# Performance work log

Hardware: AMD Instinct MI355X
Metric: run time of the kernel (lower is better)

Reference implementation:

```python
import jax, jax.numpy as jnp
import numpy as np
import math

B, T, D = 2, 1024, 256
N, H = 1024, 8
HD = N // H
K = 32
STEPS = 2
VOCAB = 32000
TWO_PI = 2.0 * math.pi


def _ln(x, g, b):
    mu = x.mean(-1, keepdims=True)
    var = ((x - mu) ** 2).mean(-1, keepdims=True)
    return (x - mu) / jnp.sqrt(var + 1e-5) * g + b


def _gelu(x):
    # torch nn.GELU default = exact erf form
    return jax.nn.gelu(x, approximate=False)


def _forward(tokens, emb, field_init, Wq, Wv, mW1, mb1, mW2, mb2, base_metric,
             decoder, hebbian, fW1, fb1, fW2, fb2, g1, b1, g2, b2, gf, bf, Wl, bl):
    x = emb[tokens] + field_init  # [B,T,D]
    # quantized RoPE (BDH): freqs quantized in pairs, phases mod 1
    freqs = 1.0 / (2.0 ** 16) ** (jnp.floor(jnp.arange(D) / 2) * 2.0 / D) / TWO_PI  # [D]
    phases = (jnp.arange(T, dtype=jnp.float32)[:, None] * freqs[None, :]) % 1.0 * TWO_PI  # [T,D]
    cos, sin = jnp.cos(phases)[None], jnp.sin(phases)[None]
    x_rot = jnp.stack([-x[..., 1::2], x[..., ::2]], axis=-1).reshape(x.shape)
    x = x * cos + x_rot * sin

    # window j of token t covers padded positions t..t+K-1 == original t-(K-1)..t (causal)
    win_idx = jnp.arange(T)[:, None] + jnp.arange(K)[None, :]  # [T,K]

    def interaction(y):
        qs = jax.nn.relu(jnp.einsum('btd,hde->bthe', y, Wq))  # [B,T,H,HD] sparse query
        vs = jax.nn.relu(jnp.einsum('btd,hde->bthe', y, Wv))  # [B,T,H,HD] sparse value
        # dynamic diagonal metric from field signature
        qf = qs.reshape(B, T, N)
        sig = qf.mean(1) + qf[:, ::8].mean(1) * 0.5  # T >= 8 branch
        mod = _gelu(sig @ mW1 + mb1) @ mW2 + mb2  # [B,H*HD]
        metric = jax.nn.softplus(base_metric[None] + 0.1 * mod.reshape(B, H, HD)) + 1e-6
        # causal k-window extraction (unfold equivalent)
        qp = jnp.pad(qs, ((0, 0), (K - 1, 0), (0, 0), (0, 0)))
        vp = jnp.pad(vs, ((0, 0), (K - 1, 0), (0, 0), (0, 0)))
        qw = qp[:, win_idx].transpose(0, 1, 3, 2, 4)  # [B,T,H,K,HD]
        vw = vp[:, win_idx].transpose(0, 1, 3, 2, 4)
        diff = qs[:, :, :, None, :] - qw
        dist = jnp.sqrt(jnp.sum(metric[:, None, :, None, :] * diff ** 2, -1) + 1e-8)  # [B,T,H,K]
        infl = jnp.exp(-dist)
        infl = infl / (infl.sum(-1, keepdims=True) + 1e-8)
        ctx = jnp.einsum('bthk,bthkd->bthd', infl, vw)
        # Hebbian memory contraction (eval mode: state is fixed buffer)
        qn = qs / jnp.maximum(jnp.linalg.norm(qs, axis=-1, keepdims=True), 1e-12)
        ctx = ctx + jnp.einsum('bthd,hde->bthe', qn, hebbian)
        # multiplicative gating + decode
        return (qs * ctx).reshape(B, T, N) @ decoder

    for _ in range(STEPS):  # fixed evolution steps (eval, dropout off)
        dx = interaction(_ln(x, g1, b1)) + (_gelu(_ln(x, g2, b2) @ fW1 + fb1) @ fW2 + fb2)
        x = x + dx
    return _ln(x, gf, bf) @ Wl + bl  # [B,T,VOCAB]


def setup_inputs() -> dict:
    key = jax.random.key(0)
    ks = jax.random.split(key, 12)
    s = 0.02
    return {
        'tokens': jax.random.randint(ks[0], (B, T), 0, VOCAB),
        'emb': jax.random.normal(ks[1], (VOCAB, D)) * s,
        'field_init': jax.random.normal(ks[2], (1, 1, D)) * s,
        'Wq': jax.random.normal(ks[3], (H, D, HD)) * s,
        'Wv': jax.random.normal(ks[4], (H, D, HD)) * s,
        'mW1': jax.random.normal(ks[5], (N, N // 2)) * s,
        'mb1': jnp.zeros((N // 2,)),
        'mW2': jax.random.normal(ks[6], (N // 2, H * HD)) * s,
        'mb2': jnp.zeros((H * HD,)),
        'base_metric': jnp.ones((H, HD)) * 0.1,
        'decoder': jax.random.normal(ks[7], (N, D)) * s,
        'hebbian': jax.random.normal(ks[8], (H, HD, HD)) * 0.01,
        'fW1': jax.random.normal(ks[9], (D, 4 * D)) * s,
        'fb1': jnp.zeros((4 * D,)),
        'fW2': jax.random.normal(ks[10], (4 * D, D)) * s,
        'fb2': jnp.zeros((D,)),
        'g1': jnp.ones((D,)), 'b1': jnp.zeros((D,)),
        'g2': jnp.ones((D,)), 'b2': jnp.zeros((D,)),
        'gf': jnp.ones((D,)), 'bf': jnp.zeros((D,)),
        'Wl': jax.random.normal(ks[11], (D, VOCAB)) * s,
        'bl': jnp.zeros((VOCAB,)),
    }


def reference(tokens, emb, field_init, Wq, Wv, mW1, mb1, mW2, mb2, base_metric,
              decoder, hebbian, fW1, fb1, fW2, fb2, g1, b1, g2, b2, gf, bf, Wl, bl):
    return _forward(tokens, emb, field_init, Wq, Wv, mW1, mb1, mW2, mb2, base_metric,
                    decoder, hebbian, fW1, fb1, fW2, fb2, g1, b1, g2, b2, gf, bf, Wl, bl)
```

## Files before the change

### kernel.cpp

```cpp
#include <hip/hip_runtime.h>
#include <hip/hip_bf16.h>
#include <math.h>

#define B_ 2
#define T_ 1024
#define D_ 256
#define N_ 1024
#define H_ 8
#define HD_ 128
#define K_ 32
#define VOCAB_ 32000

typedef __attribute__((ext_vector_type(8))) short short8v;
typedef __attribute__((ext_vector_type(4))) float f32x4;

static __device__ __forceinline__ float geluf(float x) {
    return 0.5f * x * (1.0f + erff(x * 0.70710678118654752f));
}

static __device__ __forceinline__ ushort f2bf(float f) {
    unsigned u = __builtin_bit_cast(unsigned, f);
    u += 0x7fff + ((u >> 16) & 1);
    return (ushort)(u >> 16);
}

static __device__ __forceinline__ float bf2f(ushort u) {
    unsigned v = ((unsigned)u) << 16;
    return __builtin_bit_cast(float, v);
}

__global__ void embed_rope_ln_kernel(const int* __restrict__ tokens,
                                     const float* __restrict__ emb,
                                     const float* __restrict__ field_init,
                                     const float* __restrict__ g1, const float* __restrict__ b1,
                                     const float* __restrict__ g2, const float* __restrict__ b2,
                                     float* __restrict__ x,
                                     ushort* __restrict__ y1, ushort* __restrict__ y2) {
    int bt = blockIdx.x;
    int d = threadIdx.x;
    int t = bt & (T_ - 1);
    int tok = tokens[bt];
    float v = emb[(long)tok * D_ + d] + field_init[d];
    float partner = __shfl_xor(v, 1);
    float rot = (d & 1) ? partner : -partner;
    float freq = exp2f(-0.0625f * (float)(d & ~1)) * (1.0f / 6.283185307179586f);
    float ph = fmodf((float)t * freq, 1.0f) * 6.283185307179586f;
    v = v * cosf(ph) + rot * sinf(ph);
    long i = (long)bt * D_ + d;
    x[i] = v;
    __shared__ float red[4];
    int lane = d & 63, wid = d >> 6;
    float s = v;
    #pragma unroll
    for (int off = 32; off; off >>= 1) s += __shfl_xor(s, off);
    if (lane == 0) red[wid] = s;
    __syncthreads();
    float mu = (red[0] + red[1] + red[2] + red[3]) * (1.0f / D_);
    float dv = v - mu;
    float s2 = dv * dv;
    #pragma unroll
    for (int off = 32; off; off >>= 1) s2 += __shfl_xor(s2, off);
    __syncthreads();
    if (lane == 0) red[wid] = s2;
    __syncthreads();
    float var = (red[0] + red[1] + red[2] + red[3]) * (1.0f / D_);
    float rstd = rsqrtf(var + 1e-5f);
    float nv = dv * rstd;
    y1[i] = f2bf(nv * g1[d] + b1[d]);
    y2[i] = f2bf(nv * g2[d] + b2[d]);
}

__global__ void ln_kernel(float* __restrict__ x,
                          const float* __restrict__ addA, const float* __restrict__ addB,
                          const float* __restrict__ g1, const float* __restrict__ b1,
                          const float* __restrict__ g2, const float* __restrict__ b2,
                          ushort* __restrict__ y1, ushort* __restrict__ y2) {
    int row = blockIdx.x;
    int d = threadIdx.x;
    long i = (long)row * D_ + d;
    float v = x[i] + addA[i] + addB[i];
    x[i] = v;
    __shared__ float red[4];
    int lane = d & 63, wid = d >> 6;
    float s = v;
    #pragma unroll
    for (int off = 32; off; off >>= 1) s += __shfl_xor(s, off);
    if (lane == 0) red[wid] = s;
    __syncthreads();
    float mu = (red[0] + red[1] + red[2] + red[3]) * (1.0f / D_);
    float dv = v - mu;
    float s2 = dv * dv;
    #pragma unroll
    for (int off = 32; off; off >>= 1) s2 += __shfl_xor(s2, off);
    __syncthreads();
    if (lane == 0) red[wid] = s2;
    __syncthreads();
    float var = (red[0] + red[1] + red[2] + red[3]) * (1.0f / D_);
    float rstd = rsqrtf(var + 1e-5f);
    float nv = dv * rstd;
    y1[i] = f2bf(nv * g1[d] + b1[d]);
    if (y2) y2[i] = f2bf(nv * g2[d] + b2[d]);
}

static __device__ __forceinline__ void tcast_tile(
    const float* __restrict__ in, ushort* __restrict__ out,
    int R, int C, int ry, int cx) {
    __shared__ float sm[64][65];
    int r0 = ry * 64, c0 = cx * 64;
    int tx = threadIdx.x & 63, ty = threadIdx.x >> 6;
    #pragma unroll
    for (int i = 0; i < 16; ++i) {
        int r = i * 4 + ty;
        sm[r][tx] = in[(long)(r0 + r) * C + c0 + tx];
    }
    __syncthreads();
    #pragma unroll
    for (int i = 0; i < 16; ++i) {
        int c = i * 4 + ty;
        out[(long)(c0 + c) * R + r0 + tx] = f2bf(sm[tx][c]);
    }
}

__global__ __launch_bounds__(256) void tcast_kernel(
    const float* __restrict__ in, ushort* __restrict__ out, int R, int C) {
    tcast_tile(in, out, R, C, blockIdx.y, blockIdx.x);
}

struct TcastBatch {
    const float* in[8];
    ushort* out[8];
    long inS[8], outS[8];
    int cb[8], rb[8], R[8], C[8];
    int cum[9];
};

__global__ __launch_bounds__(256) void tcast_all_kernel(TcastBatch tb) {
    int bid = blockIdx.x;
    int d = 0;
    #pragma unroll
    for (int i = 0; i < 8; ++i) if (bid >= tb.cum[i + 1]) d = i + 1;
    int local = bid - tb.cum[d];
    int bpz = tb.cb[d] * tb.rb[d];
    int z = local / bpz;
    int rem = local - z * bpz;
    int cx = rem % tb.cb[d], ry = rem / tb.cb[d];
    tcast_tile(tb.in[d] + z * tb.inS[d], tb.out[d] + z * tb.outS[d],
               tb.R[d], tb.C[d], ry, cx);
}

#define LDK 72
#define CSTR 132

template<int ACT, int OUTBF, int SIG>
__device__ __forceinline__ void gemm128_core(
    const ushort* __restrict__ A, int lda,
    const ushort* __restrict__ Bt, int ldb,
    const float* __restrict__ bias, void* __restrict__ Cout, int ldc,
    int Kd, int bx, int by,
    float* __restrict__ psOut, float* __restrict__ ps8Out) {
    __shared__ __align__(16) ushort As[128 * LDK];
    __shared__ __align__(16) ushort Bs[128 * LDK];
    int tid = threadIdx.x;
    int wid = tid >> 6, lane = tid & 63;
    int brow = by * 128, bcol = bx * 128;
    int wr = wid >> 1, wc = wid & 1;
    f32x4 acc[4][4] = {};
    for (int k0 = 0; k0 < Kd; k0 += 64) {
        __syncthreads();
        #pragma unroll
        for (int j = 0; j < 4; ++j) {
            int idx = tid + j * 256;
            int r = idx >> 3, sgm = idx & 7;
            *(short8v*)&As[r * LDK + sgm * 8] =
                *(const short8v*)&A[(long)(brow + r) * lda + k0 + sgm * 8];
            *(short8v*)&Bs[r * LDK + sgm * 8] =
                *(const short8v*)&Bt[(long)(bcol + r) * ldb + k0 + sgm * 8];
        }
        __syncthreads();
        #pragma unroll
        for (int kk = 0; kk < 2; ++kk) {
            short8v af[4], bfv[4];
            #pragma unroll
            for (int m = 0; m < 4; ++m)
                af[m] = *(const short8v*)&As[(wr * 64 + m * 16 + (lane & 15)) * LDK + kk * 32 + (lane >> 4) * 8];
            #pragma unroll
            for (int n = 0; n < 4; ++n)
                bfv[n] = *(const short8v*)&Bs[(wc * 64 + n * 16 + (lane & 15)) * LDK + kk * 32 + (lane >> 4) * 8];
            #pragma unroll
            for (int m = 0; m < 4; ++m)
                #pragma unroll
                for (int n = 0; n < 4; ++n)
                    acc[m][n] = __builtin_amdgcn_mfma_f32_16x16x32_bf16(af[m], bfv[n], acc[m][n], 0, 0, 0);
        }
    }
    float* Cs = (float*)As;
    float cs = 0.f, cs8 = 0.f;
    #pragma unroll
    for (int chunk = 0; chunk < 4; ++chunk) {
        __syncthreads();
        if (wr == (chunk >> 1)) {
            #pragma unroll
            for (int mm = 0; mm < 2; ++mm) {
                int m = (chunk & 1) * 2 + mm;
                int lr0 = mm * 16 + ((lane >> 4) << 2);
                #pragma unroll
                for (int n = 0; n < 4; ++n) {
                    int lcol = wc * 64 + n * 16 + (lane & 15);
                    #pragma unroll
                    for (int j = 0; j < 4; ++j)
                        Cs[(lr0 + j) * CSTR + lcol] = acc[m][n][j];
                }
            }
        }
        __syncthreads();
        int lrow = tid >> 3, f4 = tid & 7;
        long grow = brow + chunk * 32 + lrow;
        if (OUTBF) {
            #pragma unroll
            for (int u = 0; u < 2; ++u) {
                int c0i = (f4 + u * 8) * 8;
                uint pk[4];
                #pragma unroll
                for (int q = 0; q < 4; ++q) {
                    int cc = c0i + 2 * q;
                    float v0 = Cs[lrow * CSTR + cc]     + (bias ? bias[bcol + cc] : 0.0f);
                    float v1 = Cs[lrow * CSTR + cc + 1] + (bias ? bias[bcol + cc + 1] : 0.0f);
                    if (ACT == 1) { v0 = fmaxf(v0, 0.0f); v1 = fmaxf(v1, 0.0f); }
                    else if (ACT == 2) { v0 = geluf(v0); v1 = geluf(v1); }
                    pk[q] = (uint)f2bf(v0) | ((uint)f2bf(v1) << 16);
                }
                *(uint4*)&((ushort*)Cout)[grow * ldc + bcol + c0i] = *(uint4*)pk;
            }
        } else {
            #pragma unroll
            for (int u = 0; u < 4; ++u) {
                int c0i = (f4 + u * 8) * 4;
                float vv[4];
                #pragma unroll
                for (int q = 0; q < 4; ++q) {
                    float v = Cs[lrow * CSTR + c0i + q] + (bias ? bias[bcol + c0i + q] : 0.0f);
                    if (ACT == 1) v = fmaxf(v, 0.0f);
                    else if (ACT == 2) v = geluf(v);
                    vv[q] = v;
                }
                *(float4*)&((float*)Cout)[grow * ldc + bcol + c0i] = *(float4*)vv;
            }
        }
        if (SIG && tid < 128) {
            #pragma unroll
            for (int r = 0; r < 32; ++r) {
                float vr = fmaxf(Cs[r * CSTR + tid], 0.0f);
                cs += vr;
                if ((r & 7) == 0) cs8 += vr;
            }
        }
    }
    if (SIG && tid < 128) {
        psOut[by * 1024 + bcol + tid] = cs;
        ps8Out[by * 1024 + bcol + tid] = cs8;
    }
}

__global__ __launch_bounds__(256) void gemm3_kernel(
    const ushort* __restrict__ y1, const ushort* __restrict__ y2,
    const ushort* __restrict__ WqT, const ushort* __restrict__ WvT, const ushort* __restrict__ fW1T,
    const float* __restrict__ fb1,
    ushort* __restrict__ qs, ushort* __restrict__ vs, ushort* __restrict__ ffnh,
    float* __restrict__ ps, float* __restrict__ ps8) {
    int z = blockIdx.z;
    if (z == 0)
        gemm128_core<1, 1, 1>(y1, 256, WqT, 256, nullptr, qs, 1024, 256,
                              blockIdx.x, blockIdx.y, ps, ps8);
    else if (z == 1)
        gemm128_core<1, 1, 0>(y1, 256, WvT, 256, nullptr, vs, 1024, 256,
                              blockIdx.x, blockIdx.y, nullptr, nullptr);
    else
        gemm128_core<2, 1, 0>(y2, 256, fW1T, 256, fb1, ffnh, 1024, 256,
                              blockIdx.x, blockIdx.y, nullptr, nullptr);
}

__global__ __launch_bounds__(256) void vocab_kernel(
    const ushort* __restrict__ yf, const ushort* __restrict__ WlT,
    const float* __restrict__ bl, float* __restrict__ out) {
    int g = blockIdx.x;
    int nid = (g & 7) * 500 + (g >> 3);
    gemm128_core<0, 0, 0>(yf, 256, WlT, 256, bl, out, VOCAB_, 256,
                          nid >> 4, nid & 15, nullptr, nullptr);
}

__global__ __launch_bounds__(256) void gemm2_kernel(
    const ushort* __restrict__ gated, const ushort* __restrict__ ffnh,
    const ushort* __restrict__ decT, const ushort* __restrict__ fW2T,
    const float* __restrict__ fb2,
    float* __restrict__ dec_out, float* __restrict__ ffn_out) {
    int z = blockIdx.z;
    const ushort* A = z ? ffnh : gated;
    const ushort* Bt = z ? fW2T : decT;
    const float* bias = z ? fb2 : nullptr;
    float* C = z ? ffn_out : dec_out;
    const int Kd = 1024, N = 256;
    __shared__ __align__(16) ushort As[64 * LDK];
    __shared__ __align__(16) ushort Bs[64 * LDK];
    int tid = threadIdx.x;
    int wid = tid >> 6, lane = tid & 63;
    int brow = blockIdx.y * 64, bcol = blockIdx.x * 64;
    int wr = wid >> 1, wc = wid & 1;
    f32x4 acc[2][2] = {};
    for (int k0 = 0; k0 < Kd; k0 += 64) {
        __syncthreads();
        #pragma unroll
        for (int j = 0; j < 2; ++j) {
            int idx = tid + j * 256;
            int r = idx >> 3, sgm = idx & 7;
            *(short8v*)&As[r * LDK + sgm * 8] =
                *(const short8v*)&A[(long)(brow + r) * Kd + k0 + sgm * 8];
            *(short8v*)&Bs[r * LDK + sgm * 8] =
                *(const short8v*)&Bt[(long)(bcol + r) * Kd + k0 + sgm * 8];
        }
        __syncthreads();
        #pragma unroll
        for (int kk = 0; kk < 2; ++kk) {
            short8v af[2], bfv[2];
            #pragma unroll
            for (int m = 0; m < 2; ++m)
                af[m] = *(const short8v*)&As[(wr * 32 + m * 16 + (lane & 15)) * LDK + kk * 32 + (lane >> 4) * 8];
            #pragma unroll
            for (int n = 0; n < 2; ++n)
                bfv[n] = *(const short8v*)&Bs[(wc * 32 + n * 16 + (lane & 15)) * LDK + kk * 32 + (lane >> 4) * 8];
            #pragma unroll
            for (int m = 0; m < 2; ++m)
                #pragma unroll
                for (int n = 0; n < 2; ++n)
                    acc[m][n] = __builtin_amdgcn_mfma_f32_16x16x32_bf16(af[m], bfv[n], acc[m][n], 0, 0, 0);
        }
    }
    int r0 = brow + wr * 32 + ((lane >> 4) << 2);
    int c0 = bcol + wc * 32 + (lane & 15);
    #pragma unroll
    for (int n = 0; n < 2; ++n) {
        int col = c0 + n * 16;
        float bv = bias ? bias[col] : 0.0f;
        #pragma unroll
        for (int m = 0; m < 2; ++m)
            #pragma unroll
            for (int j = 0; j < 4; ++j)
                C[(long)(r0 + m * 16 + j) * N + col] = acc[m][n][j] + bv;
    }
}

__global__ __launch_bounds__(256) void mlp1_kernel(
    const float* __restrict__ ps, const float* __restrict__ ps8,
    const ushort* __restrict__ mW1T, const float* __restrict__ mb1,
    float* __restrict__ hid) {
    int blk = blockIdx.x;
    int b = blk >> 7;
    __shared__ float sig_l[1024];
    int tid = threadIdx.x;
    for (int c = tid; c < 1024; c += 256) {
        float s = 0.f, s8 = 0.f;
        #pragma unroll
        for (int by8 = 0; by8 < 8; ++by8) {
            s += ps[(b * 8 + by8) * 1024 + c];
            s8 += ps8[(b * 8 + by8) * 1024 + c];
        }
        sig_l[c] = s * (1.0f / 1024.0f) + 0.5f * s8 * (1.0f / 128.0f);
    }
    __syncthreads();
    int wv = tid >> 6, lane = tid & 63;
    int j = (blk & 127) * 4 + wv;
    const ushort* wrow = mW1T + (long)j * 1024;
    float acc = 0.f;
    #pragma unroll
    for (int c2 = 0; c2 < 4; ++c2) {
        int n0 = c2 * 256 + lane * 4;
        float4 sv = *(const float4*)&sig_l[n0];
        ushort4 w4 = *(const ushort4*)&wrow[n0];
        acc += bf2f(w4.x) * sv.x + bf2f(w4.y) * sv.y
             + bf2f(w4.z) * sv.z + bf2f(w4.w) * sv.w;
    }
    #pragma unroll
    for (int off = 32; off; off >>= 1) acc += __shfl_xor(acc, off);
    if (lane == 0) hid[b * 512 + j] = geluf(acc + mb1[j]);
}

__global__ __launch_bounds__(256) void mlp2_kernel(
    const float* __restrict__ hid, const ushort* __restrict__ mW2T,
    const float* __restrict__ mb2, const float* __restrict__ base_metric,
    float* __restrict__ metric) {
    int widx = blockIdx.x * 4 + (threadIdx.x >> 6);
    int b = widx >> 10, i = widx & 1023;
    int lane = threadIdx.x & 63;
    const float* hd = hid + b * 512;
    const ushort* w = mW2T + (long)i * 512;
    int j0 = lane * 8;
    short8v wv = *(const short8v*)&w[j0];
    float4 h0 = *(const float4*)&hd[j0];
    float4 h1 = *(const float4*)&hd[j0 + 4];
    float acc = bf2f((ushort)wv[0]) * h0.x + bf2f((ushort)wv[1]) * h0.y
              + bf2f((ushort)wv[2]) * h0.z + bf2f((ushort)wv[3]) * h0.w
              + bf2f((ushort)wv[4]) * h1.x + bf2f((ushort)wv[5]) * h1.y
              + bf2f((ushort)wv[6]) * h1.z + bf2f((ushort)wv[7]) * h1.w;
    #pragma unroll
    for (int off = 32; off; off >>= 1) acc += __shfl_xor(acc, off);
    if (lane == 0) {
        float v = base_metric[i] + 0.1f * (acc + mb2[i]);
        float sp = fmaxf(v, 0.f) + log1pf(expf(-fabsf(v)));
        metric[b * 1024 + i] = sp + 1e-6f;
    }
}

#define QLD 136
#define QLDU 68
#define VLD 72
#define PLD 72
#define CLD 132

__global__ __launch_bounds__(256) void window_kernel(
    const ushort* __restrict__ qs, const ushort* __restrict__ vs,
    const float* __restrict__ metric, const ushort* __restrict__ hebT,
    ushort* __restrict__ gated) {
    int tile = blockIdx.x, h = blockIdx.y, b = blockIdx.z;
    int t0 = tile * 16;
    int tid = threadIdx.x;
    __shared__ __align__(16) ushort Qt[48 * QLD];
    __shared__ __align__(16) ushort Qr[16 * QLD];
    __shared__ __align__(16) ushort Vt[128 * VLD];
    __shared__ __align__(16) ushort P[16 * PLD];
    __shared__ float ctx[16 * CLD];
    __shared__ float ns[48], invn_l[16], part[3][16], smf[128];

    if (tid < 128) smf[tid] = sqrtf(metric[(b * H_ + h) * HD_ + tid]);
    if (tid < 128) { int t = tid >> 3, c = tid & 7; ((uint*)P)[t * 36 + 24 + c] = 0; }
    __syncthreads();

    for (int i = tid; i < 48 * 64; i += 256) {
        int r = i >> 6, c = i & 63;
        int grow = t0 - 31 + r;
        uint qv = 0;
        if (r < 47 && grow >= 0)
            qv = ((const uint*)qs)[(((long)(b * T_ + grow) * N_ + h * HD_) >> 1) + c];
        float q0 = bf2f((ushort)(qv & 0xffff)) * smf[2 * c];
        float q1 = bf2f((ushort)(qv >> 16)) * smf[2 * c + 1];
        ((uint*)Qt)[r * QLDU + c] = (uint)f2bf(q0) | ((uint)f2bf(q1) << 16);
        if (r >= 31 && r < 47) ((uint*)Qr)[(r - 31) * QLDU + c] = qv;
    }
    for (int i = tid; i < 32 * 64; i += 256) {
        int r2 = i >> 6, c = i & 63;
        int ra = 2 * r2, rb_ = 2 * r2 + 1;
        int ga = t0 - 31 + ra, gb = t0 - 31 + rb_;
        uint v0 = 0, v1 = 0;
        if (ra < 47 && ga >= 0)
            v0 = ((const uint*)vs)[(((long)(b * T_ + ga) * N_ + h * HD_) >> 1) + c];
        if (rb_ < 47 && gb >= 0)
            v1 = ((const uint*)vs)[(((long)(b * T_ + gb) * N_ + h * HD_) >> 1) + c];
        ((uint*)Vt)[(2 * c) * 36 + r2]     = (v0 & 0xffff) | ((v1 & 0xffff) << 16);
        ((uint*)Vt)[(2 * c + 1) * 36 + r2] = (v0 >> 16) | (v1 & 0xffff0000u);
    }
    __syncthreads();

    int w = tid >> 6, lane = tid & 63;
    int lc = lane & 15, lr = lane >> 4;

    for (int rr = 0; rr < 16; ++rr) {
        int row = w * 16 + rr;
        uint u = (row < 48) ? ((uint*)Qt)[row * QLDU + lane]
                            : ((uint*)Qr)[(row - 48) * QLDU + lane];
        float a0 = bf2f((ushort)(u & 0xffff)), a1 = bf2f((ushort)(u >> 16));
        float nv = a0 * a0 + a1 * a1;
        #pragma unroll
        for (int off = 32; off; off >>= 1) nv += __shfl_xor(nv, off);
        if (lane == 0) {
            if (row < 48) ns[row] = nv;
            else invn_l[row - 48] = 1.0f / fmaxf(sqrtf(nv), 1e-12f);
        }
    }
    __syncthreads();

    f32x4 accS = {};
    if (w < 3) {
        #pragma unroll
        for (int k = 0; k < 4; ++k) {
            short8v a = *(const short8v*)&Qt[(w * 16 + lc) * QLD + k * 32 + lr * 8];
            short8v bf_ = *(const short8v*)&Qt[(31 + lc) * QLD + k * 32 + lr * 8];
            accS = __builtin_amdgcn_mfma_f32_16x16x32_bf16(a, bf_, accS, 0, 0, 0);
        }
    }
    f32x4 accH[2] = {};
    const ushort* hb = hebT + (long)h * HD_ * HD_;
    #pragma unroll
    for (int nt = 0; nt < 2; ++nt)
        #pragma unroll
        for (int k = 0; k < 4; ++k) {
            short8v a = *(const short8v*)&Qr[lc * QLD + k * 32 + lr * 8];
            short8v bf_ = *(const short8v*)&hb[(long)((w * 2 + nt) * 16 + lc) * HD_ + k * 32 + lr * 8];
            accH[nt] = __builtin_amdgcn_mfma_f32_16x16x32_bf16(a, bf_, accH[nt], 0, 0, 0);
        }
    #pragma unroll
    for (int nt = 0; nt < 2; ++nt)
        #pragma unroll
        for (int j = 0; j < 4; ++j) {
            int t = lr * 4 + j;
            ctx[t * CLD + (w * 2 + nt) * 16 + lc] = accH[nt][j] * invn_l[t];
        }
    float wgt[4];
    if (w < 3) {
        float nt_ = ns[31 + lc];
        float psum = 0.f;
        #pragma unroll
        for (int j = 0; j < 4; ++j) {
            int s = w * 16 + lr * 4 + j;
            float val = fmaxf(nt_ + ns[s] - 2.0f * accS[j], 0.0f) + 1e-8f;
            bool band = (s >= lc) && (s <= lc + 31);
            wgt[j] = band ? __expf(-sqrtf(val)) : 0.0f;
            psum += wgt[j];
        }
        psum += __shfl_xor(psum, 16);
        psum += __shfl_xor(psum, 32);
        if (lane < 16) part[w][lane] = psum;
    }
    __syncthreads();
    if (w < 3) {
        float inv = 1.0f / (part[0][lc] + part[1][lc] + part[2][lc] + 1e-8f);
        uint lo = (uint)f2bf(wgt[0] * inv) | ((uint)f2bf(wgt[1] * inv) << 16);
        uint hi = (uint)f2bf(wgt[2] * inv) | ((uint)f2bf(wgt[3] * inv) << 16);
        uint2 pk = {lo, hi};
        *(uint2*)&P[lc * PLD + w * 16 + lr * 4] = pk;
    }
    __syncthreads();
    f32x4 accP[2] = {};
    #pragma unroll
    for (int mt = 0; mt < 2; ++mt)
        #pragma unroll
        for (int k = 0; k < 2; ++k) {
            short8v a = *(const short8v*)&Vt[((w * 2 + mt) * 16 + lc) * VLD + k * 32 + lr * 8];
            short8v bf_ = *(const short8v*)&P[lc * PLD + k * 32 + lr * 8];
            accP[mt] = __builtin_amdgcn_mfma_f32_16x16x32_bf16(a, bf_, accP[mt], 0, 0, 0);
        }
    #pragma unroll
    for (int mt = 0; mt < 2; ++mt)
        #pragma unroll
        for (int j = 0; j < 4; ++j) {
            int e = (w * 2 + mt) * 16 + lr * 4 + j;
            ctx[lc * CLD + e] += accP[mt][j];
        }
    __syncthreads();
    {
        int t = tid >> 4, g = tid & 15;
        uint4 qu = *(const uint4*)&((const uint*)Qr)[t * QLDU + g * 4];
        const float* crow = &ctx[t * CLD + g * 8];
        uint qa[4] = {qu.x, qu.y, qu.z, qu.w};
        uint outp[4];
        #pragma unroll
        for (int q4 = 0; q4 < 4; ++q4) {
            float e0 = bf2f((ushort)(qa[q4] & 0xffff)) * crow[2 * q4];
            float e1 = bf2f((ushort)(qa[q4] >> 16))   * crow[2 * q4 + 1];
            outp[q4] = (uint)f2bf(e0) | ((uint)f2bf(e1) << 16);
        }
        *(uint4*)&gated[(long)(b * T_ + t0 + t) * N_ + h * HD_ + g * 8] = *(uint4*)outp;
    }
}

extern "C" void kernel_launch(void* const* d_in, const int* in_sizes, int n_in,
                              void* d_out, int out_size, void* d_ws, size_t ws_size,
                              hipStream_t stream) {
    const int*   tokens      = (const int*)  d_in[0];
    const float* emb         = (const float*)d_in[1];
    const float* field_init  = (const float*)d_in[2];
    const float* Wq          = (const float*)d_in[3];
    const float* Wv          = (const float*)d_in[4];
    const float* mW1         = (const float*)d_in[5];
    const float* mb1         = (const float*)d_in[6];
    const float* mW2         = (const float*)d_in[7];
    const float* mb2         = (const float*)d_in[8];
    const float* base_metric = (const float*)d_in[9];
    const float* decoder     = (const float*)d_in[10];
    const float* hebbian     = (const float*)d_in[11];
    const float* fW1         = (const float*)d_in[12];
    const float* fb1         = (const float*)d_in[13];
    const float* fW2         = (const float*)d_in[14];
    const float* fb2         = (const float*)d_in[15];
    const float* g1          = (const float*)d_in[16];
    const float* b1          = (const float*)d_in[17];
    const float* g2          = (const float*)d_in[18];
    const float* b2          = (const float*)d_in[19];
    const float* gf          = (const float*)d_in[20];
    const float* bf          = (const float*)d_in[21];
    const float* Wl          = (const float*)d_in[22];
    const float* bl          = (const float*)d_in[23];
    float* out = (float*)d_out;

    char* wp = (char*)d_ws;
    auto alloc = [&](size_t bytes) { char* p = wp; wp += (bytes + 255) & ~255UL; return p; };
    float*  x        = (float*) alloc(524288 * 4);
    ushort* y1_bf    = (ushort*)alloc(524288 * 2);
    ushort* y2_bf    = (ushort*)alloc(524288 * 2);
    ushort* yf_bf    = (ushort*)alloc(524288 * 2);
    ushort* qs_bf    = (ushort*)alloc(2097152 * 2);
    ushort* vs_bf    = (ushort*)alloc(2097152 * 2);
    ushort* gated_bf = (ushort*)alloc(2097152 * 2);
    ushort* ffnh_bf  = (ushort*)alloc(2097152 * 2);
    float*  dec_out  = (float*) alloc(524288 * 4);
    float*  ffn_out  = (float*) alloc(524288 * 4);
    ushort* WqT      = (ushort*)alloc(262144 * 2);
    ushort* WvT      = (ushort*)alloc(262144 * 2);
    ushort* decT     = (ushort*)alloc(262144 * 2);
    ushort* fW1T     = (ushort*)alloc(262144 * 2);
    ushort* fW2T     = (ushort*)alloc(262144 * 2);
    ushort* mW1T     = (ushort*)alloc(524288 * 2);
    ushort* mW2T     = (ushort*)alloc(524288 * 2);
    ushort* hebT     = (ushort*)alloc(131072 * 2);
    float*  ps       = (float*) alloc(16 * 1024 * 4);
    float*  ps8      = (float*) alloc(16 * 1024 * 4);
    float*  hid      = (float*) alloc(1024 * 4);
    float*  metricb  = (float*) alloc(2048 * 4);
    ushort* WlT      = (ushort*)qs_bf;

    TcastBatch tb;
    const float* tin[8]  = {Wq, Wv, decoder, fW1, fW2, mW1, mW2, hebbian};
    ushort*      tout[8] = {WqT, WvT, decT, fW1T, fW2T, mW1T, mW2T, hebT};
    long tinS[8]  = {256 * 128, 256 * 128, 0, 0, 0, 0, 0, 128 * 128};
    long toutS[8] = {128 * 256, 128 * 256, 0, 0, 0, 0, 0, 128 * 128};
    int tR[8] = {256, 256, 1024, 256, 1024, 1024, 512, 128};
    int tC[8] = {128, 128, 256, 1024, 256, 512, 1024, 128};
    int cum = 0;
    tb.cum[0] = 0;
    for (int i = 0; i < 8; ++i) {
        tb.in[i] = tin[i]; tb.out[i] = tout[i];
        tb.inS[i] = tinS[i]; tb.outS[i] = toutS[i];
        tb.R[i] = tR[i]; tb.C[i] = tC[i];
        tb.cb[i] = tC[i] / 64; tb.rb[i] = tR[i] / 64;
        int zc = (i == 0 || i == 1 || i == 7) ? 8 : 1;
        cum += tb.cb[i] * tb.rb[i] * zc;
        tb.cum[i + 1] = cum;
    }
    tcast_all_kernel<<<cum, 256, 0, stream>>>(tb);

    embed_rope_ln_kernel<<<B_ * T_, 256, 0, stream>>>(
        tokens, emb, field_init, g1, b1, g2, b2, x, y1_bf, y2_bf);

    for (int step = 0; step < 2; ++step) {
        if (step == 1)
            ln_kernel<<<B_ * T_, 256, 0, stream>>>(
                x, dec_out, ffn_out, g1, b1, g2, b2, y1_bf, y2_bf);
        gemm3_kernel<<<dim3(8, 16, 3), 256, 0, stream>>>(
            y1_bf, y2_bf, WqT, WvT, fW1T, fb1, qs_bf, vs_bf, ffnh_bf, ps, ps8);
        mlp1_kernel<<<256, 256, 0, stream>>>(ps, ps8, mW1T, mb1, hid);
        mlp2_kernel<<<512, 256, 0, stream>>>(hid, mW2T, mb2, base_metric, metricb);
        window_kernel<<<dim3(T_ / 16, H_, B_), 256, 0, stream>>>(
            qs_bf, vs_bf, metricb, hebT, gated_bf);
        gemm2_kernel<<<dim3(4, 32, 2), 256, 0, stream>>>(
            gated_bf, ffnh_bf, decT, fW2T, fb2, dec_out, ffn_out);
    }
    ln_kernel<<<B_ * T_, 256, 0, stream>>>(
        x, dec_out, ffn_out, gf, bf, nullptr, nullptr, yf_bf, nullptr);
    tcast_kernel<<<dim3(500, 4), 256, 0, stream>>>(Wl, WlT, 256, VOCAB_);
    vocab_kernel<<<4000, 256, 0, stream>>>(yf_bf, WlT, bl, out);
}
```

Measured before the change: 307.6 us.

## Merge prep kernels, fuse metric MLP, add nontemporal vocab stores

After: 336.4 us. +9.4%, slower.

```diff
diff --git a/kernel.cpp b/kernel.cpp
--- a/kernel.cpp
+++ b/kernel.cpp
@@ -29,45 +29,83 @@
     return __builtin_bit_cast(float, v);
 }
 
-__global__ void embed_rope_ln_kernel(const int* __restrict__ tokens,
-                                     const float* __restrict__ emb,
-                                     const float* __restrict__ field_init,
-                                     const float* __restrict__ g1, const float* __restrict__ b1,
-                                     const float* __restrict__ g2, const float* __restrict__ b2,
-                                     float* __restrict__ x,
-                                     ushort* __restrict__ y1, ushort* __restrict__ y2) {
-    int bt = blockIdx.x;
-    int d = threadIdx.x;
-    int t = bt & (T_ - 1);
-    int tok = tokens[bt];
-    float v = emb[(long)tok * D_ + d] + field_init[d];
-    float partner = __shfl_xor(v, 1);
-    float rot = (d & 1) ? partner : -partner;
-    float freq = exp2f(-0.0625f * (float)(d & ~1)) * (1.0f / 6.283185307179586f);
-    float ph = fmodf((float)t * freq, 1.0f) * 6.283185307179586f;
-    v = v * cosf(ph) + rot * sinf(ph);
-    long i = (long)bt * D_ + d;
-    x[i] = v;
-    __shared__ float red[4];
-    int lane = d & 63, wid = d >> 6;
-    float s = v;
-    #pragma unroll
-    for (int off = 32; off; off >>= 1) s += __shfl_xor(s, off);
-    if (lane == 0) red[wid] = s;
-    __syncthreads();
-    float mu = (red[0] + red[1] + red[2] + red[3]) * (1.0f / D_);
-    float dv = v - mu;
-    float s2 = dv * dv;
-    #pragma unroll
-    for (int off = 32; off; off >>= 1) s2 += __shfl_xor(s2, off);
-    __syncthreads();
-    if (lane == 0) red[wid] = s2;
-    __syncthreads();
-    float var = (red[0] + red[1] + red[2] + red[3]) * (1.0f / D_);
-    float rstd = rsqrtf(var + 1e-5f);
-    float nv = dv * rstd;
-    y1[i] = f2bf(nv * g1[d] + b1[d]);
-    y2[i] = f2bf(nv * g2[d] + b2[d]);
+struct TcastBatch {
+    const float* in[9];
+    ushort* out[9];
+    long inS[9], outS[9];
+    int cb[9], rb[9], R[9], C[9];
+    int cum[10];
+};
+
+__global__ __launch_bounds__(256) void prep_kernel(
+    TcastBatch tb,
+    const int* __restrict__ tokens, const float* __restrict__ emb,
+    const float* __restrict__ field_init,
+    const float* __restrict__ g1, const float* __restrict__ b1,
+    const float* __restrict__ g2, const float* __restrict__ b2,
+    float* __restrict__ x, ushort* __restrict__ y1, ushort* __restrict__ y2) {
+    __shared__ float sm[64][65];
+    int bid = blockIdx.x;
+    if (bid < B_ * T_) {
+        int bt = bid;
+        int d = threadIdx.x;
+        int t = bt & (T_ - 1);
+        int tok = tokens[bt];
+        float v = emb[(long)tok * D_ + d] + field_init[d];
+        float partner = __shfl_xor(v, 1);
+        float rot = (d & 1) ? partner : -partner;
+        float freq = exp2f(-0.0625f * (float)(d & ~1)) * (1.0f / 6.283185307179586f);
+        float ph = fmodf((float)t * freq, 1.0f) * 6.283185307179586f;
+        v = v * cosf(ph) + rot * sinf(ph);
+        long i = (long)bt * D_ + d;
+        x[i] = v;
+        float* red = sm[0];
+        int lane = d & 63, wid = d >> 6;
+        float s = v;
+        #pragma unroll
+        for (int off = 32; off; off >>= 1) s += __shfl_xor(s, off);
+        if (lane == 0) red[wid] = s;
+        __syncthreads();
+        float mu = (red[0] + red[1] + red[2] + red[3]) * (1.0f / D_);
+        float dv = v - mu;
+        float s2 = dv * dv;
+        #pragma unroll
+        for (int off = 32; off; off >>= 1) s2 += __shfl_xor(s2, off);
+        __syncthreads();
+        if (lane == 0) red[wid] = s2;
+        __syncthreads();
+        float var = (red[0] + red[1] + red[2] + red[3]) * (1.0f / D_);
+        float rstd = rsqrtf(var + 1e-5f);
+        float nv = dv * rstd;
+        y1[i] = f2bf(nv * g1[d] + b1[d]);
+        y2[i] = f2bf(nv * g2[d] + b2[d]);
+        return;
+    }
+    bid -= B_ * T_;
+    int dsc = 0;
+    #pragma unroll
+    for (int i = 0; i < 9; ++i) if (bid >= tb.cum[i + 1]) dsc = i + 1;
+    int local = bid - tb.cum[dsc];
+    int bpz = tb.cb[dsc] * tb.rb[dsc];
+    int z = local / bpz;
+    int rem = local - z * bpz;
+    int cx = rem % tb.cb[dsc], ry = rem / tb.cb[dsc];
+    const float* in = tb.in[dsc] + z * tb.inS[dsc];
+    ushort* out = tb.out[dsc] + z * tb.outS[dsc];
+    int R = tb.R[dsc], C = tb.C[dsc];
+    int r0 = ry * 64, c0 = cx * 64;
+    int tx = threadIdx.x & 63, ty = threadIdx.x >> 6;
+    #pragma unroll
+    for (int i = 0; i < 16; ++i) {
+        int r = i * 4 + ty;
+        sm[r][tx] = __builtin_nontemporal_load(&in[(long)(r0 + r) * C + c0 + tx]);
+    }
+    __syncthreads();
+    #pragma unroll
+    for (int i = 0; i < 16; ++i) {
+        int c = i * 4 + ty;
+        out[(long)(c0 + c) * R + r0 + tx] = f2bf(sm[tx][c]);
+    }
 }
 
 __global__ void ln_kernel(float* __restrict__ x,
@@ -102,56 +140,10 @@
     if (y2) y2[i] = f2bf(nv * g2[d] + b2[d]);
 }
 
-static __device__ __forceinline__ void tcast_tile(
-    const float* __restrict__ in, ushort* __restrict__ out,
-    int R, int C, int ry, int cx) {
-    __shared__ float sm[64][65];
-    int r0 = ry * 64, c0 = cx * 64;
-    int tx = threadIdx.x & 63, ty = threadIdx.x >> 6;
-    #pragma unroll
-    for (int i = 0; i < 16; ++i) {
-        int r = i * 4 + ty;
-        sm[r][tx] = in[(long)(r0 + r) * C + c0 + tx];
-    }
-    __syncthreads();
-    #pragma unroll
-    for (int i = 0; i < 16; ++i) {
-        int c = i * 4 + ty;
-        out[(long)(c0 + c) * R + r0 + tx] = f2bf(sm[tx][c]);
-    }
-}
-
-__global__ __launch_bounds__(256) void tcast_kernel(
-    const float* __restrict__ in, ushort* __restrict__ out, int R, int C) {
-    tcast_tile(in, out, R, C, blockIdx.y, blockIdx.x);
-}
-
-struct TcastBatch {
-    const float* in[8];
-    ushort* out[8];
-    long inS[8], outS[8];
-    int cb[8], rb[8], R[8], C[8];
-    int cum[9];
-};
-
-__global__ __launch_bounds__(256) void tcast_all_kernel(TcastBatch tb) {
-    int bid = blockIdx.x;
-    int d = 0;
-    #pragma unroll
-    for (int i = 0; i < 8; ++i) if (bid >= tb.cum[i + 1]) d = i + 1;
-    int local = bid - tb.cum[d];
-    int bpz = tb.cb[d] * tb.rb[d];
-    int z = local / bpz;
-    int rem = local - z * bpz;
-    int cx = rem % tb.cb[d], ry = rem / tb.cb[d];
-    tcast_tile(tb.in[d] + z * tb.inS[d], tb.out[d] + z * tb.outS[d],
-               tb.R[d], tb.C[d], ry, cx);
-}
-
 #define LDK 72
 #define CSTR 132
 
-template<int ACT, int OUTBF, int SIG>
+template<int ACT, int OUTBF, int SIG, int NT>
 __device__ __forceinline__ void gemm128_core(
     const ushort* __restrict__ A, int lda,
     const ushort* __restrict__ Bt, int ldb,
@@ -235,7 +227,7 @@
             #pragma unroll
             for (int u = 0; u < 4; ++u) {
                 int c0i = (f4 + u * 8) * 4;
-                float vv[4];
+                f32x4 vv;
                 #pragma unroll
                 for (int q = 0; q < 4; ++q) {
                     float v = Cs[lrow * CSTR + c0i + q] + (bias ? bias[bcol + c0i + q] : 0.0f);
@@ -243,7 +235,9 @@
                     else if (ACT == 2) v = geluf(v);
                     vv[q] = v;
                 }
-                *(float4*)&((float*)Cout)[grow * ldc + bcol + c0i] = *(float4*)vv;
+                f32x4* dst = (f32x4*)&((float*)Cout)[grow * ldc + bcol + c0i];
+                if (NT) __builtin_nontemporal_store(vv, dst);
+                else *dst = vv;
             }
         }
         if (SIG && tid < 128) {
@@ -269,14 +263,14 @@
     float* __restrict__ ps, float* __restrict__ ps8) {
     int z = blockIdx.z;
     if (z == 0)
-        gemm128_core<1, 1, 1>(y1, 256, WqT, 256, nullptr, qs, 1024, 256,
-                              blockIdx.x, blockIdx.y, ps, ps8);
+        gemm128_core<1, 1, 1, 0>(y1, 256, WqT, 256, nullptr, qs, 1024, 256,
+                                 blockIdx.x, blockIdx.y, ps, ps8);
     else if (z == 1)
-        gemm128_core<1, 1, 0>(y1, 256, WvT, 256, nullptr, vs, 1024, 256,
-                              blockIdx.x, blockIdx.y, nullptr, nullptr);
+        gemm128_core<1, 1, 0, 0>(y1, 256, WvT, 256, nullptr, vs, 1024, 256,
+                                 blockIdx.x, blockIdx.y, nullptr, nullptr);
     else
-        gemm128_core<2, 1, 0>(y2, 256, fW1T, 256, fb1, ffnh, 1024, 256,
-                              blockIdx.x, blockIdx.y, nullptr, nullptr);
+        gemm128_core<2, 1, 0, 0>(y2, 256, fW1T, 256, fb1, ffnh, 1024, 256,
+                                 blockIdx.x, blockIdx.y, nullptr, nullptr);
 }
 
 __global__ __launch_bounds__(256) void vocab_kernel(
@@ -284,8 +278,8 @@
     const float* __restrict__ bl, float* __restrict__ out) {
     int g = blockIdx.x;
     int nid = (g & 7) * 500 + (g >> 3);
-    gemm128_core<0, 0, 0>(yf, 256, WlT, 256, bl, out, VOCAB_, 256,
-                          nid >> 4, nid & 15, nullptr, nullptr);
+    gemm128_core<0, 0, 0, 1>(yf, 256, WlT, 256, bl, out, VOCAB_, 256,
+                             nid >> 4, nid & 15, nullptr, nullptr);
 }
 
 __global__ __launch_bounds__(256) void gemm2_kernel(
@@ -348,64 +342,57 @@
     }
 }
 
-__global__ __launch_bounds__(256) void mlp1_kernel(
+__global__ __launch_bounds__(1024) void mlpf_kernel(
     const float* __restrict__ ps, const float* __restrict__ ps8,
     const ushort* __restrict__ mW1T, const float* __restrict__ mb1,
-    float* __restrict__ hid) {
+    const ushort* __restrict__ mW2T, const float* __restrict__ mb2,
+    const float* __restrict__ base_metric, float* __restrict__ metric) {
     int blk = blockIdx.x;
-    int b = blk >> 7;
+    int b = blk >> 4, sub = blk & 15;
     __shared__ float sig_l[1024];
+    __shared__ float hid_l[512];
     int tid = threadIdx.x;
-    for (int c = tid; c < 1024; c += 256) {
+    {
         float s = 0.f, s8 = 0.f;
         #pragma unroll
         for (int by8 = 0; by8 < 8; ++by8) {
-            s += ps[(b * 8 + by8) * 1024 + c];
-            s8 += ps8[(b * 8 + by8) * 1024 + c];
-        }
-        sig_l[c] = s * (1.0f / 1024.0f) + 0.5f * s8 * (1.0f / 128.0f);
-    }
-    __syncthreads();
-    int wv = tid >> 6, lane = tid & 63;
-    int j = (blk & 127) * 4 + wv;
-    const ushort* wrow = mW1T + (long)j * 1024;
-    float acc = 0.f;
-    #pragma unroll
-    for (int c2 = 0; c2 < 4; ++c2) {
-        int n0 = c2 * 256 + lane * 4;
-        float4 sv = *(const float4*)&sig_l[n0];
-        ushort4 w4 = *(const ushort4*)&wrow[n0];
-        acc += bf2f(w4.x) * sv.x + bf2f(w4.y) * sv.y
-             + bf2f(w4.z) * sv.z + bf2f(w4.w) * sv.w;
-    }
-    #pragma unroll
-    for (int off = 32; off; off >>= 1) acc += __shfl_xor(acc, off);
-    if (lane == 0) hid[b * 512 + j] = geluf(acc + mb1[j]);
-}
-
-__global__ __launch_bounds__(256) void mlp2_kernel(
-    const float* __restrict__ hid, const ushort* __restrict__ mW2T,
-    const float* __restrict__ mb2, const float* __restrict__ base_metric,
-    float* __restrict__ metric) {
-    int widx = blockIdx.x * 4 + (threadIdx.x >> 6);
-    int b = widx >> 10, i = widx & 1023;
-    int lane = threadIdx.x & 63;
-    const float* hd = hid + b * 512;
-    const ushort* w = mW2T + (long)i * 512;
-    int j0 = lane * 8;
-    short8v wv = *(const short8v*)&w[j0];
-    float4 h0 = *(const float4*)&hd[j0];
-    float4 h1 = *(const float4*)&hd[j0 + 4];
-    float acc = bf2f((ushort)wv[0]) * h0.x + bf2f((ushort)wv[1]) * h0.y
-              + bf2f((ushort)wv[2]) * h0.z + bf2f((ushort)wv[3]) * h0.w
-              + bf2f((ushort)wv[4]) * h1.x + bf2f((ushort)wv[5]) * h1.y
-              + bf2f((ushort)wv[6]) * h1.z + bf2f((ushort)wv[7]) * h1.w;
-    #pragma unroll
-    for (int off = 32; off; off >>= 1) acc += __shfl_xor(acc, off);
-    if (lane == 0) {
-        float v = base_metric[i] + 0.1f * (acc + mb2[i]);
-        float sp = fmaxf(v, 0.f) + log1pf(expf(-fabsf(v)));
-        metric[b * 1024 + i] = sp + 1e-6f;
+            s += ps[(b * 8 + by8) * 1024 + tid];
+            s8 += ps8[(b * 8 + by8) * 1024 + tid];
+        }
+        sig_l[tid] = s * (1.0f / 1024.0f) + 0.5f * s8 * (1.0f / 128.0f);
+    }
+    __syncthreads();
+    int w = tid >> 6, lane = tid & 63;
+    for (int jj = 0; jj < 32; ++jj) {
+        int j = w * 32 + jj;
+        const ushort* wrow = mW1T + (long)j * 1024;
+        float acc = 0.f;
+        #pragma unroll
+        for (int e = 0; e < 16; ++e) {
+            int n = lane + 64 * e;
+            acc = fmaf(bf2f(wrow[n]), sig_l[n], acc);
+        }
+        #pragma unroll
+        for (int off = 32; off; off >>= 1) acc += __shfl_xor(acc, off);
+        if (lane == 0) hid_l[j] = geluf(acc + mb1[j]);
+    }
+    __syncthreads();
+    for (int ii = 0; ii < 4; ++ii) {
+        int i = sub * 64 + w * 4 + ii;
+        const ushort* wrow = mW2T + (long)i * 512;
+        float acc = 0.f;
+        #pragma unroll
+        for (int e = 0; e < 8; ++e) {
+            int n = lane + 64 * e;
+            acc = fmaf(bf2f(wrow[n]), hid_l[n], acc);
+        }
+        #pragma unroll
+        for (int off = 32; off; off >>= 1) acc += __shfl_xor(acc, off);
+        if (lane == 0) {
+            float v = base_metric[i] + 0.1f * (acc + mb2[i]);
+            float sp = fmaxf(v, 0.f) + log1pf(expf(-fabsf(v)));
+            metric[b * 1024 + i] = sp + 1e-6f;
+        }
     }
 }
 
@@ -430,7 +417,7 @@
     __shared__ float ns[48], invn_l[16], part[3][16], smf[128];
 
     if (tid < 128) smf[tid] = sqrtf(metric[(b * H_ + h) * HD_ + tid]);
-    if (tid < 128) { int t = tid >> 3, c = tid & 7; ((uint*)P)[t * 36 + 24 + c] = 0; }
+    if (tid < 128) { int t = tid >> 3, c = tid & 7; if (t < 16) ((uint*)P)[t * 36 + 24 + c] = 0; }
     __syncthreads();
 
     for (int i = tid; i < 48 * 64; i += 256) {
@@ -609,22 +596,21 @@
     ushort* mW1T     = (ushort*)alloc(524288 * 2);
     ushort* mW2T     = (ushort*)alloc(524288 * 2);
     ushort* hebT     = (ushort*)alloc(131072 * 2);
+    ushort* WlT      = (ushort*)alloc((size_t)VOCAB_ * 256 * 2);
     float*  ps       = (float*) alloc(16 * 1024 * 4);
     float*  ps8      = (float*) alloc(16 * 1024 * 4);
-    float*  hid      = (float*) alloc(1024 * 4);
     float*  metricb  = (float*) alloc(2048 * 4);
-    ushort* WlT      = (ushort*)qs_bf;
 
     TcastBatch tb;
-    const float* tin[8]  = {Wq, Wv, decoder, fW1, fW2, mW1, mW2, hebbian};
-    ushort*      tout[8] = {WqT, WvT, decT, fW1T, fW2T, mW1T, mW2T, hebT};
-    long tinS[8]  = {256 * 128, 256 * 128, 0, 0, 0, 0, 0, 128 * 128};
-    long toutS[8] = {128 * 256, 128 * 256, 0, 0, 0, 0, 0, 128 * 128};
-    int tR[8] = {256, 256, 1024, 256, 1024, 1024, 512, 128};
-    int tC[8] = {128, 128, 256, 1024, 256, 512, 1024, 128};
+    const float* tin[9]  = {Wq, Wv, decoder, fW1, fW2, mW1, mW2, hebbian, Wl};
+    ushort*      tout[9] = {WqT, WvT, decT, fW1T, fW2T, mW1T, mW2T, hebT, WlT};
+    long tinS[9]  = {256 * 128, 256 * 128, 0, 0, 0, 0, 0, 128 * 128, 0};
+    long toutS[9] = {128 * 256, 128 * 256, 0, 0, 0, 0, 0, 128 * 128, 0};
+    int tR[9] = {256, 256, 1024, 256, 1024, 1024, 512, 128, 256};
+    int tC[9] = {128, 128, 256, 1024, 256, 512, 1024, 128, VOCAB_};
     int cum = 0;
     tb.cum[0] = 0;
-    for (int i = 0; i < 8; ++i) {
+    for (int i = 0; i < 9; ++i) {
         tb.in[i] = tin[i]; tb.out[i] = tout[i];
         tb.inS[i] = tinS[i]; tb.outS[i] = toutS[i];
         tb.R[i] = tR[i]; tb.C[i] = tC[i];
@@ -633,10 +619,9 @@
         cum += tb.cb[i] * tb.rb[i] * zc;
         tb.cum[i + 1] = cum;
     }
-    tcast_all_kernel<<<cum, 256, 0, stream>>>(tb);
-
-    embed_rope_ln_kernel<<<B_ * T_, 256, 0, stream>>>(
-        tokens, emb, field_init, g1, b1, g2, b2, x, y1_bf, y2_bf);
+
+    prep_kernel<<<B_ * T_ + cum, 256, 0, stream>>>(
+        tb, tokens, emb, field_init, g1, b1, g2, b2, x, y1_bf, y2_bf);
 
     for (int step = 0; step < 2; ++step) {
         if (step == 1)
@@ -644,8 +629,8 @@
                 x, dec_out, ffn_out, g1, b1, g2, b2, y1_bf, y2_bf);
         gemm3_kernel<<<dim3(8, 16, 3), 256, 0, stream>>>(
             y1_bf, y2_bf, WqT, WvT, fW1T, fb1, qs_bf, vs_bf, ffnh_bf, ps, ps8);
-        mlp1_kernel<<<256, 256, 0, stream>>>(ps, ps8, mW1T, mb1, hid);
-        mlp2_kernel<<<512, 256, 0, stream>>>(hid, mW2T, mb2, base_metric, metricb);
+        mlpf_kernel<<<32, 1024, 0, stream>>>(
+            ps, ps8, mW1T, mb1, mW2T, mb2, base_metric, metricb);
         window_kernel<<<dim3(T_ / 16, H_, B_), 256, 0, stream>>>(
             qs_bf, vs_bf, metricb, hebT, gated_bf);
         gemm2_kernel<<<dim3(4, 32, 2), 256, 0, stream>>>(
@@ -653,6 +638,5 @@
     }
     ln_kernel<<<B_ * T_, 256, 0, stream>>>(
         x, dec_out, ffn_out, gf, bf, nullptr, nullptr, yf_bf, nullptr);
-    tcast_kernel<<<dim3(500, 4), 256, 0, stream>>>(Wl, WlT, 256, VOCAB_);
     vocab_kernel<<<4000, 256, 0, stream>>>(yf_bf, WlT, bl, out);
 }
```
